# Optimization experiments

Hardware: AMD Instinct MI355X
Metric: run time of the kernel (lower is better)

The kernel has to match this reference:

```python
import jax, jax.numpy as jnp
import numpy as np

D = 256; NH = 8; NLEV = 4; NPTS = 4; DH = D // NH
DFFN = 1024; B = 8; LQ = 900
SHAPES = np.array([[100, 100], [50, 50], [25, 25], [13, 13]], dtype=np.int64)
STARTS = np.concatenate([[0], np.cumsum(SHAPES[:, 0] * SHAPES[:, 1])[:-1]]).astype(np.int64)
LEN = int((SHAPES[:, 0] * SHAPES[:, 1]).sum())


def _ln(x, w, b, eps=1e-5):
    m = x.mean(-1, keepdims=True)
    v = ((x - m) ** 2).mean(-1, keepdims=True)
    return (x - m) / jnp.sqrt(v + eps) * w + b


def _msdeform(q, ref, src, val_w, val_b, off_w, off_b, aw_w, aw_b, op_w, op_b):
    # Multi-scale deformable attention (Deformable DETR core), grid_sample
    # bilinear / zeros padding / align_corners=False semantics.
    Bq, Lq = q.shape[0], q.shape[1]
    value = (src @ val_w + val_b).reshape(Bq, -1, NH, DH)
    off = (q @ off_w + off_b).reshape(Bq, Lq, NH, NLEV, NPTS, 2)
    aw = jax.nn.softmax((q @ aw_w + aw_b).reshape(Bq, Lq, NH, NLEV * NPTS), -1)
    aw = aw.reshape(Bq, Lq, NH, NLEV, NPTS)
    norm = jnp.asarray(SHAPES[:, ::-1].copy(), dtype=q.dtype)  # (W_l, H_l)
    loc = ref[:, :, None, :, None, :] + off / norm[None, None, None, :, None, :]
    out = jnp.zeros((Bq, Lq, NH, DH), q.dtype)
    for l in range(NLEV):
        Hl, Wl = int(SHAPES[l, 0]), int(SHAPES[l, 1]); s = int(STARTS[l])
        v = value[:, s:s + Hl * Wl]                  # [B, Hl*Wl, NH, DH]
        lx = loc[:, :, :, l, :, 0] * Wl - 0.5        # align_corners=False pixel coords
        ly = loc[:, :, :, l, :, 1] * Hl - 0.5        # [B, Lq, NH, NPTS]
        x0 = jnp.floor(lx); y0 = jnp.floor(ly)
        fx = lx - x0; fy = ly - y0
        x0 = x0.astype(jnp.int32); y0 = y0.astype(jnp.int32)
        samp = jnp.zeros((Bq, Lq, NH, NPTS, DH), q.dtype)
        for dx, dy in ((0, 0), (1, 0), (0, 1), (1, 1)):
            xi = x0 + dx; yi = y0 + dy
            w = (fx if dx else 1.0 - fx) * (fy if dy else 1.0 - fy)
            valid = (xi >= 0) & (xi < Wl) & (yi >= 0) & (yi < Hl)
            idx = jnp.clip(yi, 0, Hl - 1) * Wl + jnp.clip(xi, 0, Wl - 1)
            idx_f = idx.transpose(0, 1, 3, 2).reshape(Bq, Lq * NPTS, NH)
            g = jnp.take_along_axis(v, idx_f[..., None], axis=1)
            g = g.reshape(Bq, Lq, NPTS, NH, DH).transpose(0, 1, 3, 2, 4)
            samp = samp + jnp.where(valid, w, 0.0)[..., None] * g
        out = out + jnp.sum(samp * aw[:, :, :, l, :, None], axis=3)
    return out.reshape(Bq, Lq, D) @ op_w + op_b


def _forward(tgt, query_pos, reference_points, src, qkv_w, qkv_b, out_w, out_b,
             ln2_w, ln2_b, val_w, val_b, off_w, off_b, aw_w, aw_b, op_w, op_b,
             ln1_w, ln1_b, w1, b1, w2, b2, ln3_w, ln3_b):
    Bq, Lq, _ = tgt.shape
    # --- self attention: q=k=tgt+pos, value=tgt (eval mode, no dropout) ---
    q = tgt + query_pos
    wq, wk, wv = qkv_w[:, :D], qkv_w[:, D:2 * D], qkv_w[:, 2 * D:]
    bq, bk, bv = qkv_b[:D], qkv_b[D:2 * D], qkv_b[2 * D:]
    qh = (q @ wq + bq).reshape(Bq, Lq, NH, DH)
    kh = (q @ wk + bk).reshape(Bq, Lq, NH, DH)
    vh = (tgt @ wv + bv).reshape(Bq, Lq, NH, DH)
    scores = jnp.einsum('bqhd,bkhd->bhqk', qh, kh) / jnp.sqrt(jnp.asarray(DH, tgt.dtype))
    attn = jax.nn.softmax(scores, -1)
    sa = jnp.einsum('bhqk,bkhd->bqhd', attn, vh).reshape(Bq, Lq, D) @ out_w + out_b
    tgt = _ln(tgt + sa, ln2_w, ln2_b)
    # --- multi-scale deformable cross attention ---
    ca = _msdeform(tgt + query_pos, reference_points, src,
                   val_w, val_b, off_w, off_b, aw_w, aw_b, op_w, op_b)
    tgt = _ln(tgt + ca, ln1_w, ln1_b)
    # --- FFN ---
    ff = jax.nn.relu(tgt @ w1 + b1) @ w2 + b2
    return _ln(tgt + ff, ln3_w, ln3_b)


def setup_inputs():
    key = jax.random.key(0)
    ks = jax.random.split(key, 16)
    s = 0.02
    return {
        'tgt': jax.random.normal(ks[0], (B, LQ, D), jnp.float32),
        'query_pos': jax.random.normal(ks[1], (B, LQ, D), jnp.float32),
        'reference_points': jax.random.uniform(ks[2], (B, LQ, NLEV, 2), jnp.float32),
        'src': jax.random.normal(ks[3], (B, LEN, D), jnp.float32),
        'spatial_shapes': jnp.asarray(SHAPES),
        'level_start_index': jnp.asarray(STARTS),
        'qkv_w': jax.random.normal(ks[4], (D, 3 * D), jnp.float32) * s,
        'qkv_b': jnp.zeros((3 * D,), jnp.float32),
        'out_w': jax.random.normal(ks[5], (D, D), jnp.float32) * s,
        'out_b': jnp.zeros((D,), jnp.float32),
        'ln2_w': jnp.ones((D,), jnp.float32), 'ln2_b': jnp.zeros((D,), jnp.float32),
        'val_w': jax.random.normal(ks[6], (D, D), jnp.float32) * s,
        'val_b': jnp.zeros((D,), jnp.float32),
        'off_w': jax.random.normal(ks[7], (D, NH * NLEV * NPTS * 2), jnp.float32) * s,
        'off_b': jax.random.normal(ks[8], (NH * NLEV * NPTS * 2,), jnp.float32) * 0.5,
        'aw_w': jax.random.normal(ks[9], (D, NH * NLEV * NPTS), jnp.float32) * s,
        'aw_b': jnp.zeros((NH * NLEV * NPTS,), jnp.float32),
        'op_w': jax.random.normal(ks[10], (D, D), jnp.float32) * s,
        'op_b': jnp.zeros((D,), jnp.float32),
        'ln1_w': jnp.ones((D,), jnp.float32), 'ln1_b': jnp.zeros((D,), jnp.float32),
        'w1': jax.random.normal(ks[11], (D, DFFN), jnp.float32) * s,
        'b1': jnp.zeros((DFFN,), jnp.float32),
        'w2': jax.random.normal(ks[12], (DFFN, D), jnp.float32) * s,
        'b2': jnp.zeros((D,), jnp.float32),
        'ln3_w': jnp.ones((D,), jnp.float32), 'ln3_b': jnp.zeros((D,), jnp.float32),
    }


def reference(tgt, query_pos, reference_points, src, spatial_shapes, level_start_index,
              qkv_w, qkv_b, out_w, out_b, ln2_w, ln2_b, val_w, val_b, off_w, off_b,
              aw_w, aw_b, op_w, op_b, ln1_w, ln1_b, w1, b1, w2, b2, ln3_w, ln3_b):
    return _forward(tgt, query_pos, reference_points, src, qkv_w, qkv_b, out_w, out_b,
                    ln2_w, ln2_b, val_w, val_b, off_w, off_b, aw_w, aw_b, op_w, op_b,
                    ln1_w, ln1_b, w1, b1, w2, b2, ln3_w, ln3_b)
```

## Files before the change

kernel.cpp:

```cpp
#include <hip/hip_runtime.h>
#include <math.h>

#define Dm    256
#define NHm   8
#define DHm   32
#define NLEVm 4
#define NPTSm 4
#define DFFNm 1024
#define Bm    8
#define LQm   900
#define LENm  13294
#define MQ    (Bm * LQm)
#define MV    (Bm * LENm)
#define MQP   7296
#define MVP   106368
#define LQP   960

typedef __attribute__((ext_vector_type(8))) short short8;
typedef __attribute__((ext_vector_type(4))) float f32x4;

__device__ __forceinline__ unsigned short f2bf(float f) {
    unsigned int b = __float_as_uint(f);
    unsigned int r = (b + 0x7FFFu + ((b >> 16) & 1u)) >> 16;
    return (unsigned short)r;
}
__device__ __forceinline__ float bf2f(unsigned short u) {
    return __uint_as_float(((unsigned int)u) << 16);
}

__global__ __launch_bounds__(256) void prep0(const float* __restrict__ tgt,
                                             const float* __restrict__ qpos,
                                             unsigned short* __restrict__ tgtb,
                                             unsigned short* __restrict__ qb,
                                             int n4, int n4pad) {
    int i = blockIdx.x * blockDim.x + threadIdx.x;
    int stride = gridDim.x * blockDim.x;
    for (; i < n4pad; i += stride) {
        ushort4 ut, uq;
        if (i < n4) {
            float4 x = reinterpret_cast<const float4*>(tgt)[i];
            float4 y = reinterpret_cast<const float4*>(qpos)[i];
            ut.x = f2bf(x.x); ut.y = f2bf(x.y); ut.z = f2bf(x.z); ut.w = f2bf(x.w);
            uq.x = f2bf(x.x + y.x); uq.y = f2bf(x.y + y.y);
            uq.z = f2bf(x.z + y.z); uq.w = f2bf(x.w + y.w);
        } else {
            ut.x = ut.y = ut.z = ut.w = 0;
            uq.x = uq.y = uq.z = uq.w = 0;
        }
        reinterpret_cast<ushort4*>(tgtb)[i] = ut;
        reinterpret_cast<ushort4*>(qb)[i] = uq;
    }
}

__device__ __forceinline__ void wt_tile(const float* __restrict__ W,
                                        unsigned short* __restrict__ BT,
                                        int N, int K, int n0, int k0, int t,
                                        float (*tile)[65]) {
    #pragma unroll
    for (int r0 = 0; r0 < 64; r0 += 16) {
        int r = r0 + (t >> 4);
        int c = (t & 15) * 4;
        float4 v = *reinterpret_cast<const float4*>(W + (size_t)(k0 + r) * N + n0 + c);
        tile[r][c + 0] = v.x; tile[r][c + 1] = v.y; tile[r][c + 2] = v.z; tile[r][c + 3] = v.w;
    }
    __syncthreads();
    #pragma unroll
    for (int s = t; s < 512; s += 256) {
        int r = s >> 3, c8 = (s & 7) * 8;
        short8 u;
        #pragma unroll
        for (int j = 0; j < 8; ++j) u[j] = (short)f2bf(tile[c8 + j][r]);
        *reinterpret_cast<short8*>(BT + (size_t)(n0 + r) * K + k0 + c8) = u;
    }
}

__global__ __launch_bounds__(256) void wt_all(
        const float* __restrict__ qkv_w, const float* __restrict__ out_w,
        const float* __restrict__ val_w, const float* __restrict__ off_w,
        const float* __restrict__ aw_w,  const float* __restrict__ op_w,
        const float* __restrict__ w1,    const float* __restrict__ w2,
        unsigned short* __restrict__ BT_qkv, unsigned short* __restrict__ BT_out,
        unsigned short* __restrict__ BT_val, unsigned short* __restrict__ BT_off,
        unsigned short* __restrict__ BT_aw,  unsigned short* __restrict__ BT_op,
        unsigned short* __restrict__ BT_w1,  unsigned short* __restrict__ BT_w2) {
    __shared__ float tile[64][65];
    int bid = blockIdx.x;
    int t = threadIdx.x;
    const float* W; unsigned short* BT; int N, K, idx;
    if      (bid < 48)  { W = qkv_w; BT = BT_qkv; N = 768;  K = 256;  idx = bid; }
    else if (bid < 64)  { W = out_w; BT = BT_out; N = 256;  K = 256;  idx = bid - 48; }
    else if (bid < 80)  { W = val_w; BT = BT_val; N = 256;  K = 256;  idx = bid - 64; }
    else if (bid < 96)  { W = off_w; BT = BT_off; N = 256;  K = 256;  idx = bid - 80; }
    else if (bid < 104) { W = aw_w;  BT = BT_aw;  N = 128;  K = 256;  idx = bid - 96; }
    else if (bid < 120) { W = op_w;  BT = BT_op;  N = 256;  K = 256;  idx = bid - 104; }
    else if (bid < 184) { W = w1;    BT = BT_w1;  N = 1024; K = 256;  idx = bid - 120; }
    else                { W = w2;    BT = BT_w2;  N = 256;  K = 1024; idx = bid - 184; }
    int nt = N / 64;
    int n0 = (idx % nt) * 64, k0 = (idx / nt) * 64;
    wt_tile(W, BT, N, K, n0, k0, t, tile);
}

__device__ __forceinline__ void mfma_step(const unsigned short* Ac, const unsigned short* Bc,
                                          int wr, int wc, int l, f32x4 acc[4][4]) {
    short8 af[4], bfr[4];
    #pragma unroll
    for (int m = 0; m < 4; ++m)
        af[m] = *(const short8*)(Ac + (wr + m * 16 + (l & 15)) * 32 + (l >> 4) * 8);
    #pragma unroll
    for (int n = 0; n < 4; ++n)
        bfr[n] = *(const short8*)(Bc + (wc + n * 16 + (l & 15)) * 32 + (l >> 4) * 8);
    #pragma unroll
    for (int m = 0; m < 4; ++m)
        #pragma unroll
        for (int n = 0; n < 4; ++n)
            acc[m][n] = __builtin_amdgcn_mfma_f32_16x16x32_bf16(af[m], bfr[n], acc[m][n], 0, 0, 0);
}

template <int RELU, int OBF>
__global__ __launch_bounds__(256) void bgemm(int M, int N, int K,
        const unsigned short* __restrict__ A,
        const unsigned short* __restrict__ BT,
        const float* __restrict__ bias, const float* __restrict__ bias2,
        float* __restrict__ Cf, float* __restrict__ Cf2,
        unsigned short* __restrict__ Cb, int ldc) {
    __shared__ __align__(16) unsigned short As[2][128 * 32];
    __shared__ __align__(16) unsigned short Bs[2][128 * 32];
    int t = threadIdx.x;
    int l = t & 63;
    int w = t >> 6;
    int row0 = blockIdx.x * 128, col0 = blockIdx.y * 128;
    int wr = (w >> 1) * 64, wc = (w & 1) * 64;
    f32x4 acc[4][4];
    #pragma unroll
    for (int m = 0; m < 4; ++m)
        #pragma unroll
        for (int n = 0; n < 4; ++n) acc[m][n] = (f32x4){0.f, 0.f, 0.f, 0.f};

    int s0 = t, s1 = t + 256;
    const unsigned short* Ag = A + (size_t)row0 * K;
    const unsigned short* Bg = BT + (size_t)col0 * K;
    const unsigned short* a0p = Ag + (size_t)(s0 >> 2) * K + (s0 & 3) * 8;
    const unsigned short* a1p = Ag + (size_t)(s1 >> 2) * K + (s1 & 3) * 8;
    const unsigned short* b0p = Bg + (size_t)(s0 >> 2) * K + (s0 & 3) * 8;
    const unsigned short* b1p = Bg + (size_t)(s1 >> 2) * K + (s1 & 3) * 8;

    short8 ra0 = *(const short8*)(a0p);
    short8 ra1 = *(const short8*)(a1p);
    short8 rb0 = *(const short8*)(b0p);
    short8 rb1 = *(const short8*)(b1p);

    int cur = 0;
    for (int k0 = 0; k0 < K; k0 += 32) {
        unsigned short* Ac = As[cur];
        unsigned short* Bc = Bs[cur];
        *(short8*)(Ac + s0 * 8) = ra0;
        *(short8*)(Ac + s1 * 8) = ra1;
        *(short8*)(Bc + s0 * 8) = rb0;
        *(short8*)(Bc + s1 * 8) = rb1;
        if (k0 + 32 < K) {
            ra0 = *(const short8*)(a0p + k0 + 32);
            ra1 = *(const short8*)(a1p + k0 + 32);
            rb0 = *(const short8*)(b0p + k0 + 32);
            rb1 = *(const short8*)(b1p + k0 + 32);
        }
        __syncthreads();
        mfma_step(Ac, Bc, wr, wc, l, acc);
        cur ^= 1;
    }

    int cr = (l >> 4) * 4;
    int cc = l & 15;
    #pragma unroll
    for (int m = 0; m < 4; ++m) {
        #pragma unroll
        for (int n = 0; n < 4; ++n) {
            int col = col0 + wc + n * 16 + cc;
            if (OBF == 3) {
                float bv = (col < 256) ? bias[col] : bias2[col - 256];
                #pragma unroll
                for (int j = 0; j < 4; ++j) {
                    int r = row0 + wr + m * 16 + cr + j;
                    if (r < M) {
                        float v = acc[m][n][j] + bv;
                        if (col < 256) Cf[(size_t)r * 256 + col] = v;
                        else           Cf2[(size_t)r * 128 + (col - 256)] = v;
                    }
                }
            } else {
                float bv = bias[col];
                #pragma unroll
                for (int j = 0; j < 4; ++j) {
                    int r = row0 + wr + m * 16 + cr + j;
                    if (r < M) {
                        float v = acc[m][n][j] + bv;
                        if (RELU) v = fmaxf(v, 0.f);
                        if (OBF) Cb[(size_t)r * ldc + col] = f2bf(v);
                        else     Cf[(size_t)r * ldc + col] = v;
                    }
                }
            }
        }
    }
}

__global__ __launch_bounds__(256) void fused_gemms(
        const float* __restrict__ src, const unsigned short* __restrict__ BT_val,
        const float* __restrict__ val_b, unsigned short* __restrict__ value_bf,
        const unsigned short* __restrict__ Qbf, const unsigned short* __restrict__ BT_qkv,
        const float* __restrict__ qkv_b, unsigned short* __restrict__ qk_bf,
        const unsigned short* __restrict__ tgt_bf, unsigned short* __restrict__ Vt) {
    __shared__ __align__(16) unsigned short As[2][128 * 32];
    __shared__ __align__(16) unsigned short Bs[2][128 * 32];
    int bid = blockIdx.x;
    int t = threadIdx.x;

    if (bid >= 2004) {
        int i = (bid - 2004) * 256 + t;
        int row = i / 60, c = 900 + (i % 60);
        Vt[(size_t)row * LQP + c] = 0;
        return;
    }

    int l = t & 63, w = t >> 6;
    int wr = (w >> 1) * 64, wc = (w & 1) * 64;
    int s0 = t, s1 = t + 256;
    f32x4 acc[4][4];
    #pragma unroll
    for (int m = 0; m < 4; ++m)
        #pragma unroll
        for (int n = 0; n < 4; ++n) acc[m][n] = (f32x4){0.f, 0.f, 0.f, 0.f};
    int cr = (l >> 4) * 4;
    int cc = l & 15;

    if (bid < 1662) {
        int row0 = (bid % 831) * 128, col0 = (bid / 831) * 128;
        int r0c = min(row0 + (s0 >> 2), MV - 1);
        int r1c = min(row0 + (s1 >> 2), MV - 1);
        const float* a0p = src + (size_t)r0c * 256 + (s0 & 3) * 8;
        const float* a1p = src + (size_t)r1c * 256 + (s1 & 3) * 8;
        const unsigned short* Bg = BT_val + (size_t)col0 * 256;
        const unsigned short* b0p = Bg + (size_t)(s0 >> 2) * 256 + (s0 & 3) * 8;
        const unsigned short* b1p = Bg + (size_t)(s1 >> 2) * 256 + (s1 & 3) * 8;

        float4 fa0 = *(const float4*)(a0p);
        float4 fa1 = *(const float4*)(a0p + 4);
        float4 fb0 = *(const float4*)(a1p);
        float4 fb1 = *(const float4*)(a1p + 4);
        short8 rb0 = *(const short8*)(b0p);
        short8 rb1 = *(const short8*)(b1p);

        int cur = 0;
        for (int k0 = 0; k0 < 256; k0 += 32) {
            unsigned short* Ac = As[cur];
            unsigned short* Bc = Bs[cur];
            short8 ra0, ra1;
            ra0[0] = (short)f2bf(fa0.x); ra0[1] = (short)f2bf(fa0.y);
            ra0[2] = (short)f2bf(fa0.z); ra0[3] = (short)f2bf(fa0.w);
            ra0[4] = (short)f2bf(fa1.x); ra0[5] = (short)f2bf(fa1.y);
            ra0[6] = (short)f2bf(fa1.z); ra0[7] = (short)f2bf(fa1.w);
            ra1[0] = (short)f2bf(fb0.x); ra1[1] = (short)f2bf(fb0.y);
            ra1[2] = (short)f2bf(fb0.z); ra1[3] = (short)f2bf(fb0.w);
            ra1[4] = (short)f2bf(fb1.x); ra1[5] = (short)f2bf(fb1.y);
            ra1[6] = (short)f2bf(fb1.z); ra1[7] = (short)f2bf(fb1.w);
            *(short8*)(Ac + s0 * 8) = ra0;
            *(short8*)(Ac + s1 * 8) = ra1;
            *(short8*)(Bc + s0 * 8) = rb0;
            *(short8*)(Bc + s1 * 8) = rb1;
            if (k0 + 32 < 256) {
                fa0 = *(const float4*)(a0p + k0 + 32);
                fa1 = *(const float4*)(a0p + k0 + 36);
                fb0 = *(const float4*)(a1p + k0 + 32);
                fb1 = *(const float4*)(a1p + k0 + 36);
                rb0 = *(const short8*)(b0p + k0 + 32);
                rb1 = *(const short8*)(b1p + k0 + 32);
            }
            __syncthreads();
            mfma_step(Ac, Bc, wr, wc, l, acc);
            cur ^= 1;
        }
        #pragma unroll
        for (int m = 0; m < 4; ++m) {
            #pragma unroll
            for (int n = 0; n < 4; ++n) {
                int col = col0 + wc + n * 16 + cc;
                float bv = val_b[col];
                #pragma unroll
                for (int j = 0; j < 4; ++j) {
                    int r = row0 + wr + m * 16 + cr + j;
                    if (r < MV)
                        value_bf[(size_t)r * 256 + col] = f2bf(acc[m][n][j] + bv);
                }
            }
        }
    } else {
        bool is_qk = (bid < 1890);
        int idx = is_qk ? (bid - 1662) : (bid - 1890);
        int row0 = (idx % 57) * 128;
        int col0 = (idx / 57) * 128;
        const unsigned short* A  = is_qk ? Qbf : tgt_bf;
        const unsigned short* BT = is_qk ? BT_qkv : (BT_qkv + 512 * 256);
        const float* bias        = is_qk ? qkv_b : (qkv_b + 512);

        const unsigned short* Ag = A + (size_t)row0 * 256;
        const unsigned short* Bg = BT + (size_t)col0 * 256;
        const unsigned short* a0p = Ag + (size_t)(s0 >> 2) * 256 + (s0 & 3) * 8;
        const unsigned short* a1p = Ag + (size_t)(s1 >> 2) * 256 + (s1 & 3) * 8;
        const unsigned short* b0p = Bg + (size_t)(s0 >> 2) * 256 + (s0 & 3) * 8;
        const unsigned short* b1p = Bg + (size_t)(s1 >> 2) * 256 + (s1 & 3) * 8;

        short8 ra0 = *(const short8*)(a0p);
        short8 ra1 = *(const short8*)(a1p);
        short8 rb0 = *(const short8*)(b0p);
        short8 rb1 = *(const short8*)(b1p);

        int cur = 0;
        for (int k0 = 0; k0 < 256; k0 += 32) {
            unsigned short* Ac = As[cur];
            unsigned short* Bc = Bs[cur];
            *(short8*)(Ac + s0 * 8) = ra0;
            *(short8*)(Ac + s1 * 8) = ra1;
            *(short8*)(Bc + s0 * 8) = rb0;
            *(short8*)(Bc + s1 * 8) = rb1;
            if (k0 + 32 < 256) {
                ra0 = *(const short8*)(a0p + k0 + 32);
                ra1 = *(const short8*)(a1p + k0 + 32);
                rb0 = *(const short8*)(b0p + k0 + 32);
                rb1 = *(const short8*)(b1p + k0 + 32);
            }
            __syncthreads();
            mfma_step(Ac, Bc, wr, wc, l, acc);
            cur ^= 1;
        }

        if (is_qk) {
            #pragma unroll
            for (int m = 0; m < 4; ++m) {
                #pragma unroll
                for (int n = 0; n < 4; ++n) {
                    int col = col0 + wc + n * 16 + cc;
                    float bv = bias[col];
                    #pragma unroll
                    for (int j = 0; j < 4; ++j) {
                        int r = row0 + wr + m * 16 + cr + j;
                        if (r < MQ)
                            qk_bf[(size_t)r * 512 + col] = f2bf(acc[m][n][j] + bv);
                    }
                }
            }
        } else {
            #pragma unroll
            for (int m = 0; m < 4; ++m) {
                #pragma unroll
                for (int n = 0; n < 4; ++n) {
                    int col = col0 + wc + n * 16 + cc;
                    float bv = bias[col];
                    int r0 = row0 + wr + m * 16 + cr;
                    if (r0 < MQ) {
                        int bb = r0 / 900;
                        int q = r0 - bb * 900;
                        ushort4 u;
                        u.x = f2bf(acc[m][n][0] + bv);
                        u.y = f2bf(acc[m][n][1] + bv);
                        u.z = f2bf(acc[m][n][2] + bv);
                        u.w = f2bf(acc[m][n][3] + bv);
                        *reinterpret_cast<ushort4*>(Vt + ((size_t)(bb * 256 + col)) * LQP + q) = u;
                    }
                }
            }
        }
    }
}

__global__ __launch_bounds__(256) void flash_mfma(const unsigned short* __restrict__ qk,
                                                  const unsigned short* __restrict__ vt,
                                                  unsigned short* __restrict__ out) {
    __shared__ unsigned short P_lds[4][16][72];
    int t = threadIdx.x;
    int l = t & 63, w = t >> 6;
    int lr = l & 15, lg = l >> 4;
    int qt = blockIdx.x, h = blockIdx.y, b = blockIdx.z;
    const float scale = 0.17677669529663687f;

    short8 qf = *(const short8*)(qk + (size_t)(b * LQm + qt * 64 + w * 16 + lr) * 512 + h * 32 + lg * 8);

    f32x4 accO[2];
    accO[0] = (f32x4){0.f, 0.f, 0.f, 0.f};
    accO[1] = (f32x4){0.f, 0.f, 0.f, 0.f};
    float mrow[4] = {-1e30f, -1e30f, -1e30f, -1e30f};
    float lrow[4] = {0.f, 0.f, 0.f, 0.f};
    const f32x4 zero = (f32x4){0.f, 0.f, 0.f, 0.f};
    const unsigned short* vtb = vt + ((size_t)(b * 256 + h * 32)) * LQP;

    for (int kt = 0; kt < 15; ++kt) {
        int k0 = kt * 64;
        f32x4 sfr[4];
        #pragma unroll
        for (int ks = 0; ks < 4; ++ks) {
            short8 kf = *(const short8*)(qk + (size_t)(b * LQm + k0 + ks * 16 + lr) * 512 + 256 + h * 32 + lg * 8);
            sfr[ks] = __builtin_amdgcn_mfma_f32_16x16x32_bf16(qf, kf, zero, 0, 0, 0);
        }
        float sv[4][4];
        #pragma unroll
        for (int ks = 0; ks < 4; ++ks) {
            bool valid = (k0 + ks * 16 + lr) < LQm;
            #pragma unroll
            for (int j = 0; j < 4; ++j)
                sv[ks][j] = valid ? sfr[ks][j] * scale : -1e30f;
        }
        float tm[4], newm[4], rr[4], ps[4];
        #pragma unroll
        for (int j = 0; j < 4; ++j)
            tm[j] = fmaxf(fmaxf(sv[0][j], sv[1][j]), fmaxf(sv[2][j], sv[3][j]));
        #pragma unroll
        for (int msk = 1; msk <= 8; msk <<= 1) {
            #pragma unroll
            for (int j = 0; j < 4; ++j) tm[j] = fmaxf(tm[j], __shfl_xor(tm[j], msk));
        }
        #pragma unroll
        for (int j = 0; j < 4; ++j) {
            newm[j] = fmaxf(mrow[j], tm[j]);
            rr[j] = __expf(mrow[j] - newm[j]);
            mrow[j] = newm[j];
            ps[j] = 0.f;
        }
        float pv[4][4];
        #pragma unroll
        for (int ks = 0; ks < 4; ++ks)
            #pragma unroll
            for (int j = 0; j < 4; ++j) {
                pv[ks][j] = __expf(sv[ks][j] - newm[j]);
                ps[j] += pv[ks][j];
            }
        #pragma unroll
        for (int msk = 1; msk <= 8; msk <<= 1) {
            #pragma unroll
            for (int j = 0; j < 4; ++j) ps[j] += __shfl_xor(ps[j], msk);
        }
        #pragma unroll
        for (int j = 0; j < 4; ++j) lrow[j] = lrow[j] * rr[j] + ps[j];
        #pragma unroll
        for (int n = 0; n < 2; ++n)
            #pragma unroll
            for (int j = 0; j < 4; ++j) accO[n][j] *= rr[j];
        #pragma unroll
        for (int ks = 0; ks < 4; ++ks)
            #pragma unroll
            for (int j = 0; j < 4; ++j)
                P_lds[w][lg * 4 + j][ks * 16 + lr] = f2bf(pv[ks][j]);
        #pragma unroll
        for (int kh2 = 0; kh2 < 2; ++kh2) {
            short8 pf = *(const short8*)(&P_lds[w][lr][kh2 * 32 + lg * 8]);
            #pragma unroll
            for (int n = 0; n < 2; ++n) {
                short8 vf = *(const short8*)(vtb + (size_t)(n * 16 + lr) * LQP + k0 + kh2 * 32 + lg * 8);
                accO[n] = __builtin_amdgcn_mfma_f32_16x16x32_bf16(pf, vf, accO[n], 0, 0, 0);
            }
        }
    }
    float inv[4];
    #pragma unroll
    for (int j = 0; j < 4; ++j) inv[j] = 1.0f / lrow[j];
    #pragma unroll
    for (int n = 0; n < 2; ++n)
        #pragma unroll
        for (int j = 0; j < 4; ++j) {
            int q = qt * 64 + w * 16 + lg * 4 + j;
            if (q < LQm)
                out[(size_t)(b * LQm + q) * 256 + h * 32 + n * 16 + lr] = f2bf(accO[n][j] * inv[j]);
        }
}

template <int DUAL, int QP>
__global__ __launch_bounds__(256) void add_ln_kernel(const float* __restrict__ x,
                                                     const float* __restrict__ r,
                                                     const float* __restrict__ w,
                                                     const float* __restrict__ b,
                                                     const float* __restrict__ qpos,
                                                     float* __restrict__ out,
                                                     unsigned short* __restrict__ outb,
                                                     unsigned short* __restrict__ outq) {
    int row = blockIdx.x * 4 + (threadIdx.x >> 6);
    int lane = threadIdx.x & 63;
    size_t i4 = (size_t)row * 64 + lane;
    float4 xv = reinterpret_cast<const float4*>(x)[i4];
    float4 rv = reinterpret_cast<const float4*>(r)[i4];
    float4 v = make_float4(xv.x + rv.x, xv.y + rv.y, xv.z + rv.z, xv.w + rv.w);
    float s = v.x + v.y + v.z + v.w;
    #pragma unroll
    for (int msk = 1; msk <= 32; msk <<= 1) s += __shfl_xor(s, msk);
    float mean = s * (1.0f / Dm);
    float4 dv = make_float4(v.x - mean, v.y - mean, v.z - mean, v.w - mean);
    float sq = dv.x * dv.x + dv.y * dv.y + dv.z * dv.z + dv.w * dv.w;
    #pragma unroll
    for (int msk = 1; msk <= 32; msk <<= 1) sq += __shfl_xor(sq, msk);
    float is = rsqrtf(sq * (1.0f / Dm) + 1e-5f);
    float4 wv = reinterpret_cast<const float4*>(w)[lane];
    float4 bv = reinterpret_cast<const float4*>(b)[lane];
    float4 res = make_float4(dv.x * is * wv.x + bv.x, dv.y * is * wv.y + bv.y,
                             dv.z * is * wv.z + bv.z, dv.w * is * wv.w + bv.w);
    reinterpret_cast<float4*>(out)[i4] = res;
    if (DUAL) {
        ushort4 u;
        u.x = f2bf(res.x); u.y = f2bf(res.y); u.z = f2bf(res.z); u.w = f2bf(res.w);
        reinterpret_cast<ushort4*>(outb)[i4] = u;
    }
    if (QP) {
        float4 qv = reinterpret_cast<const float4*>(qpos)[i4];
        ushort4 u;
        u.x = f2bf(res.x + qv.x); u.y = f2bf(res.y + qv.y);
        u.z = f2bf(res.z + qv.z); u.w = f2bf(res.w + qv.w);
        reinterpret_cast<ushort4*>(outq)[i4] = u;
    }
}

__global__ __launch_bounds__(256) void msdeform_kernel(const unsigned short* __restrict__ value,
                                                       const float* __restrict__ ref,
                                                       const float* __restrict__ off,
                                                       const float* __restrict__ awl,
                                                       unsigned short* __restrict__ out) {
    const int HL[4] = {100, 50, 25, 13};
    const int ST[4] = {0, 10000, 12500, 13125};
    __shared__ float lsx[4][128], lsy[4][128], wtab[4][128];
    __shared__ float2 ctab[4][512];
    int wv = threadIdx.x >> 6, lane = threadIdx.x & 63;
    int m = blockIdx.x * 4 + wv;
    int b = m / LQm;

    #pragma unroll
    for (int e = lane; e < 128; e += 64) {
        int lev = (e >> 2) & 3;
        float rx = ref[((size_t)m * NLEVm + lev) * 2 + 0];
        float ry = ref[((size_t)m * NLEVm + lev) * 2 + 1];
        float ox = off[(size_t)m * 256 + e * 2 + 0];
        float oy = off[(size_t)m * 256 + e * 2 + 1];
        float Wf = (float)HL[lev];
        lsx[wv][e] = (rx + ox / Wf) * Wf - 0.5f;
        lsy[wv][e] = (ry + oy / Wf) * Wf - 0.5f;
        wtab[wv][e] = awl[(size_t)m * 128 + e];
    }
    __syncthreads();
    if (lane < NHm) {
        int h = lane;
        float mx = -1e30f;
        #pragma unroll
        for (int i = 0; i < 16; i++) mx = fmaxf(mx, wtab[wv][h * 16 + i]);
        float s = 0.f;
        #pragma unroll
        for (int i = 0; i < 16; i++) {
            float e = __expf(wtab[wv][h * 16 + i] - mx);
            wtab[wv][h * 16 + i] = e; s += e;
        }
        float inv = 1.0f / s;
        #pragma unroll
        for (int i = 0; i < 16; i++) wtab[wv][h * 16 + i] *= inv;
    }
    __syncthreads();
    #pragma unroll
    for (int j = 0; j < 8; ++j) {
        int e2 = lane * 8 + j;
        int c = e2 & 3, e = e2 >> 2;
        int lev = (e >> 2) & 3;
        int Wl = HL[lev];
        float lx = lsx[wv][e], ly = lsy[wv][e];
        float x0f = floorf(lx), y0f = floorf(ly);
        float fx = lx - x0f, fy = ly - y0f;
        int dx = c & 1, dy = c >> 1;
        int xi = (int)x0f + dx, yi = (int)y0f + dy;
        bool valid = (xi >= 0) && (xi < Wl) && (yi >= 0) && (yi < Wl);
        float wc = valid ? ((dx ? fx : 1.0f - fx) * (dy ? fy : 1.0f - fy)) * wtab[wv][e] : 0.f;
        int xc = min(max(xi, 0), Wl - 1), yc = min(max(yi, 0), Wl - 1);
        int row = b * LENm + ST[lev] + yc * Wl + xc;
        ctab[wv][e2] = make_float2(__int_as_float(row), wc);
    }
    __syncthreads();
    int h = lane >> 3, dg = lane & 7;
    const unsigned short* basep = value + h * 32 + dg * 4;
    float a0 = 0.f, a1 = 0.f, a2 = 0.f, a3 = 0.f;
    #pragma unroll
    for (int i = 0; i < 16; ++i) {
        #pragma unroll
        for (int c = 0; c < 4; ++c) {
            float2 cc = ctab[wv][(h * 16 + i) * 4 + c];
            int row = __float_as_int(cc.x);
            float wc = cc.y;
            ushort4 v = *reinterpret_cast<const ushort4*>(basep + (size_t)row * 256);
            a0 += wc * bf2f(v.x); a1 += wc * bf2f(v.y);
            a2 += wc * bf2f(v.z); a3 += wc * bf2f(v.w);
        }
    }
    ushort4 o;
    o.x = f2bf(a0); o.y = f2bf(a1); o.z = f2bf(a2); o.w = f2bf(a3);
    *reinterpret_cast<ushort4*>(out + (size_t)m * 256 + h * 32 + dg * 4) = o;
}

extern "C" void kernel_launch(void* const* d_in, const int* in_sizes, int n_in,
                              void* d_out, int out_size, void* d_ws, size_t ws_size,
                              hipStream_t stream) {
    const float* tgt   = (const float*)d_in[0];
    const float* qpos  = (const float*)d_in[1];
    const float* refp  = (const float*)d_in[2];
    const float* src   = (const float*)d_in[3];
    const float* qkv_w = (const float*)d_in[6];
    const float* qkv_b = (const float*)d_in[7];
    const float* out_w = (const float*)d_in[8];
    const float* out_b = (const float*)d_in[9];
    const float* ln2_w = (const float*)d_in[10];
    const float* ln2_b = (const float*)d_in[11];
    const float* val_w = (const float*)d_in[12];
    const float* val_b = (const float*)d_in[13];
    const float* off_w = (const float*)d_in[14];
    const float* off_b = (const float*)d_in[15];
    const float* aw_w  = (const float*)d_in[16];
    const float* aw_b  = (const float*)d_in[17];
    const float* op_w  = (const float*)d_in[18];
    const float* op_b  = (const float*)d_in[19];
    const float* ln1_w = (const float*)d_in[20];
    const float* ln1_b = (const float*)d_in[21];
    const float* w1    = (const float*)d_in[22];
    const float* b1    = (const float*)d_in[23];
    const float* w2    = (const float*)d_in[24];
    const float* b2    = (const float*)d_in[25];
    const float* ln3_w = (const float*)d_in[26];
    const float* ln3_b = (const float*)d_in[27];

    char* base = (char*)d_ws;
    unsigned short* value_bf  = (unsigned short*)(base);
    unsigned short* hidden_bf = (unsigned short*)(base + 54460416);
    unsigned short* t2_bf     = (unsigned short*)(base + 54460416 + 14942208);
    unsigned short* qk_bf = (unsigned short*)(base + 108920832);
    float* offb = (float*)(base + 108920832);
    float* awb  = (float*)(base + 108920832 + 7372800);
    unsigned short* Vt = (unsigned short*)(base + 123666432);
    float* S1   = (float*)(base + 123666432);
    float* t1   = (float*)(base + 131039232);
    float* t2   = (float*)(base + 138412032);
    unsigned short* Qbf     = (unsigned short*)(base + 145784832);
    unsigned short* tgt_bf  = (unsigned short*)(base + 149520384);
    unsigned short* attn_bf = (unsigned short*)(base + 153255936);
    unsigned short* ca_bf   = (unsigned short*)(base + 156991488);
    unsigned short* BT_qkv  = (unsigned short*)(base + 160727040);
    unsigned short* BT_out  = BT_qkv + 768 * 256;
    unsigned short* BT_val  = BT_out + 256 * 256;
    unsigned short* BT_off  = BT_val + 256 * 256;
    unsigned short* BT_aw   = BT_off + 256 * 256;
    unsigned short* BT_op   = BT_aw + 128 * 256;
    unsigned short* BT_w1   = BT_op + 256 * 256;
    unsigned short* BT_w2   = BT_w1 + 1024 * 256;
    float* outp = (float*)d_out;

    dim3 blk(256);
    wt_all<<<dim3(248), blk, 0, stream>>>(qkv_w, out_w, val_w, off_w, aw_w, op_w, w1, w2,
                                          BT_qkv, BT_out, BT_val, BT_off, BT_aw, BT_op, BT_w1, BT_w2);
    prep0<<<dim3(1824), blk, 0, stream>>>(tgt, qpos, tgt_bf, Qbf, MQ * Dm / 4, MQP * Dm / 4);

    fused_gemms<<<dim3(2484), blk, 0, stream>>>(src, BT_val, val_b, value_bf,
                                                Qbf, BT_qkv, qkv_b, qk_bf, tgt_bf, Vt);

    flash_mfma<<<dim3(15, NHm, Bm), blk, 0, stream>>>(qk_bf, Vt, attn_bf);
    bgemm<0, 0><<<dim3(57, 2), blk, 0, stream>>>(MQ, 256, 256, attn_bf, BT_out, out_b, nullptr, S1, nullptr, nullptr, 256);
    add_ln_kernel<0, 1><<<dim3(1800), blk, 0, stream>>>(tgt, S1, ln2_w, ln2_b, qpos, t1, nullptr, Qbf);
    bgemm<0, 3><<<dim3(57, 3), blk, 0, stream>>>(MQ, 384, 256, Qbf, BT_off, off_b, aw_b, offb, awb, nullptr, 0);
    msdeform_kernel<<<dim3(1800), blk, 0, stream>>>(value_bf, refp, offb, awb, ca_bf);
    bgemm<0, 0><<<dim3(57, 2), blk, 0, stream>>>(MQ, 256, 256, ca_bf, BT_op, op_b, nullptr, S1, nullptr, nullptr, 256);
    add_ln_kernel<1, 0><<<dim3(1800), blk, 0, stream>>>(t1, S1, ln1_w, ln1_b, nullptr, t2, t2_bf, nullptr);
    bgemm<1, 1><<<dim3(57, 8), blk, 0, stream>>>(MQ, DFFNm, 256, t2_bf, BT_w1, b1, nullptr, nullptr, nullptr, hidden_bf, DFFNm);
    bgemm<0, 0><<<dim3(57, 2), blk, 0, stream>>>(MQ, 256, 1024, hidden_bf, BT_w2, b2, nullptr, S1, nullptr, nullptr, 256);
    add_ln_kernel<0, 0><<<dim3(1800), blk, 0, stream>>>(t2, S1, ln3_w, ln3_b, nullptr, outp, nullptr, nullptr);
}
```

Before: 251.4 us.

## Overlap value projection with self-attention chain via staged combo kernels

Splits the large value-projection GEMM (src @ val_w) into chunks and co-schedules each chunk inside a sequence of combo kernel launches. The same launches also run the self-attention pipeline stages: QKV projection, flash attention, out-projection, LN plus query_pos, and the offset/attention-weight GEMM. The goal is to fill idle CUs during the small, low-occupancy self-attention stages with independent value-GEMM tiles, and to fold the weight transpose and the input prep into one launch. The cost is a more complex heterogeneous block dispatch and a shared LDS size that may limit occupancy.

```diff
diff --git a/kernel.cpp b/kernel.cpp
--- a/kernel.cpp
+++ b/kernel.cpp
@@ -28,16 +28,46 @@
     return __uint_as_float(((unsigned int)u) << 16);
 }
 
-__global__ __launch_bounds__(256) void prep0(const float* __restrict__ tgt,
-                                             const float* __restrict__ qpos,
-                                             unsigned short* __restrict__ tgtb,
-                                             unsigned short* __restrict__ qb,
-                                             int n4, int n4pad) {
-    int i = blockIdx.x * blockDim.x + threadIdx.x;
-    int stride = gridDim.x * blockDim.x;
-    for (; i < n4pad; i += stride) {
+__device__ __forceinline__ void wt_tile(const float* __restrict__ W,
+                                        unsigned short* __restrict__ BT,
+                                        int N, int K, int n0, int k0, int t,
+                                        float (*tile)[65]) {
+    #pragma unroll
+    for (int r0 = 0; r0 < 64; r0 += 16) {
+        int r = r0 + (t >> 4);
+        int c = (t & 15) * 4;
+        float4 v = *reinterpret_cast<const float4*>(W + (size_t)(k0 + r) * N + n0 + c);
+        tile[r][c + 0] = v.x; tile[r][c + 1] = v.y; tile[r][c + 2] = v.z; tile[r][c + 3] = v.w;
+    }
+    __syncthreads();
+    #pragma unroll
+    for (int s = t; s < 512; s += 256) {
+        int r = s >> 3, c8 = (s & 7) * 8;
+        short8 u;
+        #pragma unroll
+        for (int j = 0; j < 8; ++j) u[j] = (short)f2bf(tile[c8 + j][r]);
+        *reinterpret_cast<short8*>(BT + (size_t)(n0 + r) * K + k0 + c8) = u;
+    }
+}
+
+__global__ __launch_bounds__(256) void wt_prep(
+        const float* __restrict__ qkv_w, const float* __restrict__ out_w,
+        const float* __restrict__ val_w, const float* __restrict__ off_w,
+        const float* __restrict__ aw_w,  const float* __restrict__ op_w,
+        const float* __restrict__ w1,    const float* __restrict__ w2,
+        unsigned short* __restrict__ BT_qkv, unsigned short* __restrict__ BT_out,
+        unsigned short* __restrict__ BT_val, unsigned short* __restrict__ BT_off,
+        unsigned short* __restrict__ BT_aw,  unsigned short* __restrict__ BT_op,
+        unsigned short* __restrict__ BT_w1,  unsigned short* __restrict__ BT_w2,
+        const float* __restrict__ tgt, const float* __restrict__ qpos,
+        unsigned short* __restrict__ tgtb, unsigned short* __restrict__ qb) {
+    __shared__ float tile[64][65];
+    int bid = blockIdx.x;
+    int t = threadIdx.x;
+    if (bid >= 248) {
+        int i = (bid - 248) * 256 + t;
         ushort4 ut, uq;
-        if (i < n4) {
+        if (i < MQ * 64) {
             float4 x = reinterpret_cast<const float4*>(tgt)[i];
             float4 y = reinterpret_cast<const float4*>(qpos)[i];
             ut.x = f2bf(x.x); ut.y = f2bf(x.y); ut.z = f2bf(x.z); ut.w = f2bf(x.w);
@@ -49,43 +79,8 @@
         }
         reinterpret_cast<ushort4*>(tgtb)[i] = ut;
         reinterpret_cast<ushort4*>(qb)[i] = uq;
-    }
-}
-
-__device__ __forceinline__ void wt_tile(const float* __restrict__ W,
-                                        unsigned short* __restrict__ BT,
-                                        int N, int K, int n0, int k0, int t,
-                                        float (*tile)[65]) {
-    #pragma unroll
-    for (int r0 = 0; r0 < 64; r0 += 16) {
-        int r = r0 + (t >> 4);
-        int c = (t & 15) * 4;
-        float4 v = *reinterpret_cast<const float4*>(W + (size_t)(k0 + r) * N + n0 + c);
-        tile[r][c + 0] = v.x; tile[r][c + 1] = v.y; tile[r][c + 2] = v.z; tile[r][c + 3] = v.w;
-    }
-    __syncthreads();
-    #pragma unroll
-    for (int s = t; s < 512; s += 256) {
-        int r = s >> 3, c8 = (s & 7) * 8;
-        short8 u;
-        #pragma unroll
-        for (int j = 0; j < 8; ++j) u[j] = (short)f2bf(tile[c8 + j][r]);
-        *reinterpret_cast<short8*>(BT + (size_t)(n0 + r) * K + k0 + c8) = u;
-    }
-}
-
-__global__ __launch_bounds__(256) void wt_all(
-        const float* __restrict__ qkv_w, const float* __restrict__ out_w,
-        const float* __restrict__ val_w, const float* __restrict__ off_w,
-        const float* __restrict__ aw_w,  const float* __restrict__ op_w,
-        const float* __restrict__ w1,    const float* __restrict__ w2,
-        unsigned short* __restrict__ BT_qkv, unsigned short* __restrict__ BT_out,
-        unsigned short* __restrict__ BT_val, unsigned short* __restrict__ BT_off,
-        unsigned short* __restrict__ BT_aw,  unsigned short* __restrict__ BT_op,
-        unsigned short* __restrict__ BT_w1,  unsigned short* __restrict__ BT_w2) {
-    __shared__ float tile[64][65];
-    int bid = blockIdx.x;
-    int t = threadIdx.x;
+        return;
+    }
     const float* W; unsigned short* BT; int N, K, idx;
     if      (bid < 48)  { W = qkv_w; BT = BT_qkv; N = 768;  K = 256;  idx = bid; }
     else if (bid < 64)  { W = out_w; BT = BT_out; N = 256;  K = 256;  idx = bid - 48; }
@@ -100,8 +95,8 @@
     wt_tile(W, BT, N, K, n0, k0, t, tile);
 }
 
-__device__ __forceinline__ void mfma_step(const unsigned short* Ac, const unsigned short* Bc,
-                                          int wr, int wc, int l, f32x4 acc[4][4]) {
+__device__ __forceinline__ void mfma_tilestep(const unsigned short* Ac, const unsigned short* Bc,
+                                              int wr, int wc, int l, f32x4 acc[4][4]) {
     short8 af[4], bfr[4];
     #pragma unroll
     for (int m = 0; m < 4; ++m)
@@ -114,15 +109,380 @@
         #pragma unroll
         for (int n = 0; n < 4; ++n)
             acc[m][n] = __builtin_amdgcn_mfma_f32_16x16x32_bf16(af[m], bfr[n], acc[m][n], 0, 0, 0);
+}
+
+__device__ __forceinline__ void bf16_mainloop(int t, const unsigned short* __restrict__ Ag,
+                                              const unsigned short* __restrict__ Bg,
+                                              unsigned short* Sh, f32x4 acc[4][4]) {
+    int l = t & 63, w = t >> 6;
+    int wr = (w >> 1) * 64, wc = (w & 1) * 64;
+    int s0 = t, s1 = t + 256;
+    const unsigned short* a0p = Ag + (size_t)(s0 >> 2) * 256 + (s0 & 3) * 8;
+    const unsigned short* a1p = Ag + (size_t)(s1 >> 2) * 256 + (s1 & 3) * 8;
+    const unsigned short* b0p = Bg + (size_t)(s0 >> 2) * 256 + (s0 & 3) * 8;
+    const unsigned short* b1p = Bg + (size_t)(s1 >> 2) * 256 + (s1 & 3) * 8;
+    short8 ra0 = *(const short8*)(a0p);
+    short8 ra1 = *(const short8*)(a1p);
+    short8 rb0 = *(const short8*)(b0p);
+    short8 rb1 = *(const short8*)(b1p);
+    int cur = 0;
+    for (int k0 = 0; k0 < 256; k0 += 32) {
+        unsigned short* Ac = Sh + cur * 4096;
+        unsigned short* Bc = Sh + 8192 + cur * 4096;
+        *(short8*)(Ac + s0 * 8) = ra0;
+        *(short8*)(Ac + s1 * 8) = ra1;
+        *(short8*)(Bc + s0 * 8) = rb0;
+        *(short8*)(Bc + s1 * 8) = rb1;
+        if (k0 + 32 < 256) {
+            ra0 = *(const short8*)(a0p + k0 + 32);
+            ra1 = *(const short8*)(a1p + k0 + 32);
+            rb0 = *(const short8*)(b0p + k0 + 32);
+            rb1 = *(const short8*)(b1p + k0 + 32);
+        }
+        __syncthreads();
+        mfma_tilestep(Ac, Bc, wr, wc, l, acc);
+        cur ^= 1;
+    }
+}
+
+__device__ __forceinline__ void value_tile(int vbid, int t, const float* __restrict__ src,
+        const unsigned short* __restrict__ BT_val, const float* __restrict__ val_b,
+        unsigned short* __restrict__ value_bf, unsigned short* Sh) {
+    int l = t & 63, w = t >> 6;
+    int wr = (w >> 1) * 64, wc = (w & 1) * 64;
+    int row0 = (vbid % 831) * 128, col0 = (vbid / 831) * 128;
+    f32x4 acc[4][4];
+    #pragma unroll
+    for (int m = 0; m < 4; ++m)
+        #pragma unroll
+        for (int n = 0; n < 4; ++n) acc[m][n] = (f32x4){0.f, 0.f, 0.f, 0.f};
+    int s0 = t, s1 = t + 256;
+    int r0c = min(row0 + (s0 >> 2), MV - 1);
+    int r1c = min(row0 + (s1 >> 2), MV - 1);
+    const float* a0p = src + (size_t)r0c * 256 + (s0 & 3) * 8;
+    const float* a1p = src + (size_t)r1c * 256 + (s1 & 3) * 8;
+    const unsigned short* Bg = BT_val + (size_t)col0 * 256;
+    const unsigned short* b0p = Bg + (size_t)(s0 >> 2) * 256 + (s0 & 3) * 8;
+    const unsigned short* b1p = Bg + (size_t)(s1 >> 2) * 256 + (s1 & 3) * 8;
+    float4 fa0 = *(const float4*)(a0p);
+    float4 fa1 = *(const float4*)(a0p + 4);
+    float4 fb0 = *(const float4*)(a1p);
+    float4 fb1 = *(const float4*)(a1p + 4);
+    short8 rb0 = *(const short8*)(b0p);
+    short8 rb1 = *(const short8*)(b1p);
+    int cur = 0;
+    for (int k0 = 0; k0 < 256; k0 += 32) {
+        unsigned short* Ac = Sh + cur * 4096;
+        unsigned short* Bc = Sh + 8192 + cur * 4096;
+        short8 ra0, ra1;
+        ra0[0] = (short)f2bf(fa0.x); ra0[1] = (short)f2bf(fa0.y);
+        ra0[2] = (short)f2bf(fa0.z); ra0[3] = (short)f2bf(fa0.w);
+        ra0[4] = (short)f2bf(fa1.x); ra0[5] = (short)f2bf(fa1.y);
+        ra0[6] = (short)f2bf(fa1.z); ra0[7] = (short)f2bf(fa1.w);
+        ra1[0] = (short)f2bf(fb0.x); ra1[1] = (short)f2bf(fb0.y);
+        ra1[2] = (short)f2bf(fb0.z); ra1[3] = (short)f2bf(fb0.w);
+        ra1[4] = (short)f2bf(fb1.x); ra1[5] = (short)f2bf(fb1.y);
+        ra1[6] = (short)f2bf(fb1.z); ra1[7] = (short)f2bf(fb1.w);
+        *(short8*)(Ac + s0 * 8) = ra0;
+        *(short8*)(Ac + s1 * 8) = ra1;
+        *(short8*)(Bc + s0 * 8) = rb0;
+        *(short8*)(Bc + s1 * 8) = rb1;
+        if (k0 + 32 < 256) {
+            fa0 = *(const float4*)(a0p + k0 + 32);
+            fa1 = *(const float4*)(a0p + k0 + 36);
+            fb0 = *(const float4*)(a1p + k0 + 32);
+            fb1 = *(const float4*)(a1p + k0 + 36);
+            rb0 = *(const short8*)(b0p + k0 + 32);
+            rb1 = *(const short8*)(b1p + k0 + 32);
+        }
+        __syncthreads();
+        mfma_tilestep(Ac, Bc, wr, wc, l, acc);
+        cur ^= 1;
+    }
+    int cr = (l >> 4) * 4, cc = l & 15;
+    #pragma unroll
+    for (int m = 0; m < 4; ++m) {
+        #pragma unroll
+        for (int n = 0; n < 4; ++n) {
+            int col = col0 + wc + n * 16 + cc;
+            float bv = val_b[col];
+            #pragma unroll
+            for (int j = 0; j < 4; ++j) {
+                int r = row0 + wr + m * 16 + cr + j;
+                if (r < MV)
+                    value_bf[(size_t)r * 256 + col] = f2bf(acc[m][n][j] + bv);
+            }
+        }
+    }
+}
+
+__device__ __forceinline__ void flash_block(int sid, int t,
+        const unsigned short* __restrict__ qk, const unsigned short* __restrict__ vt,
+        unsigned short* __restrict__ out, unsigned short* P_lds ) {
+    int l = t & 63, w = t >> 6;
+    int lr = l & 15, lg = l >> 4;
+    int qt = sid % 15, h = (sid / 15) % 8, b = sid / 120;
+    const float scale = 0.17677669529663687f;
+    unsigned short* Pw = P_lds + w * 1152;
+
+    short8 qf = *(const short8*)(qk + (size_t)(b * LQm + qt * 64 + w * 16 + lr) * 512 + h * 32 + lg * 8);
+
+    f32x4 accO[2];
+    accO[0] = (f32x4){0.f, 0.f, 0.f, 0.f};
+    accO[1] = (f32x4){0.f, 0.f, 0.f, 0.f};
+    float mrow[4] = {-1e30f, -1e30f, -1e30f, -1e30f};
+    float lrow[4] = {0.f, 0.f, 0.f, 0.f};
+    const f32x4 zero = (f32x4){0.f, 0.f, 0.f, 0.f};
+    const unsigned short* vtb = vt + ((size_t)(b * 256 + h * 32)) * LQP;
+
+    for (int kt = 0; kt < 15; ++kt) {
+        int k0 = kt * 64;
+        f32x4 sfr[4];
+        #pragma unroll
+        for (int ks = 0; ks < 4; ++ks) {
+            short8 kf = *(const short8*)(qk + (size_t)(b * LQm + k0 + ks * 16 + lr) * 512 + 256 + h * 32 + lg * 8);
+            sfr[ks] = __builtin_amdgcn_mfma_f32_16x16x32_bf16(qf, kf, zero, 0, 0, 0);
+        }
+        float sv[4][4];
+        #pragma unroll
+        for (int ks = 0; ks < 4; ++ks) {
+            bool valid = (k0 + ks * 16 + lr) < LQm;
+            #pragma unroll
+            for (int j = 0; j < 4; ++j)
+                sv[ks][j] = valid ? sfr[ks][j] * scale : -1e30f;
+        }
+        float tm[4], newm[4], rr[4], ps[4];
+        #pragma unroll
+        for (int j = 0; j < 4; ++j)
+            tm[j] = fmaxf(fmaxf(sv[0][j], sv[1][j]), fmaxf(sv[2][j], sv[3][j]));
+        #pragma unroll
+        for (int msk = 1; msk <= 8; msk <<= 1) {
+            #pragma unroll
+            for (int j = 0; j < 4; ++j) tm[j] = fmaxf(tm[j], __shfl_xor(tm[j], msk));
+        }
+        #pragma unroll
+        for (int j = 0; j < 4; ++j) {
+            newm[j] = fmaxf(mrow[j], tm[j]);
+            rr[j] = __expf(mrow[j] - newm[j]);
+            mrow[j] = newm[j];
+            ps[j] = 0.f;
+        }
+        float pv[4][4];
+        #pragma unroll
+        for (int ks = 0; ks < 4; ++ks)
+            #pragma unroll
+            for (int j = 0; j < 4; ++j) {
+                pv[ks][j] = __expf(sv[ks][j] - newm[j]);
+                ps[j] += pv[ks][j];
+            }
+        #pragma unroll
+        for (int msk = 1; msk <= 8; msk <<= 1) {
+            #pragma unroll
+            for (int j = 0; j < 4; ++j) ps[j] += __shfl_xor(ps[j], msk);
+        }
+        #pragma unroll
+        for (int j = 0; j < 4; ++j) lrow[j] = lrow[j] * rr[j] + ps[j];
+        #pragma unroll
+        for (int n = 0; n < 2; ++n)
+            #pragma unroll
+            for (int j = 0; j < 4; ++j) accO[n][j] *= rr[j];
+        #pragma unroll
+        for (int ks = 0; ks < 4; ++ks)
+            #pragma unroll
+            for (int j = 0; j < 4; ++j)
+                Pw[(lg * 4 + j) * 72 + ks * 16 + lr] = f2bf(pv[ks][j]);
+        #pragma unroll
+        for (int kh2 = 0; kh2 < 2; ++kh2) {
+            short8 pf = *(const short8*)(Pw + lr * 72 + kh2 * 32 + lg * 8);
+            #pragma unroll
+            for (int n = 0; n < 2; ++n) {
+                short8 vf = *(const short8*)(vtb + (size_t)(n * 16 + lr) * LQP + k0 + kh2 * 32 + lg * 8);
+                accO[n] = __builtin_amdgcn_mfma_f32_16x16x32_bf16(pf, vf, accO[n], 0, 0, 0);
+            }
+        }
+    }
+    float inv[4];
+    #pragma unroll
+    for (int j = 0; j < 4; ++j) inv[j] = 1.0f / lrow[j];
+    #pragma unroll
+    for (int n = 0; n < 2; ++n)
+        #pragma unroll
+        for (int j = 0; j < 4; ++j) {
+            int q = qt * 64 + w * 16 + lg * 4 + j;
+            if (q < LQm)
+                out[(size_t)(b * LQm + q) * 256 + h * 32 + n * 16 + lr] = f2bf(accO[n][j] * inv[j]);
+        }
+}
+
+__device__ __forceinline__ void ln_block(int sid, int t, const float* __restrict__ x,
+        const float* __restrict__ r, const float* __restrict__ w, const float* __restrict__ b,
+        const float* __restrict__ qpos, float* __restrict__ out,
+        unsigned short* __restrict__ outq) {
+    int row = sid * 4 + (t >> 6);
+    int lane = t & 63;
+    size_t i4 = (size_t)row * 64 + lane;
+    float4 xv = reinterpret_cast<const float4*>(x)[i4];
+    float4 rv = reinterpret_cast<const float4*>(r)[i4];
+    float4 v = make_float4(xv.x + rv.x, xv.y + rv.y, xv.z + rv.z, xv.w + rv.w);
+    float s = v.x + v.y + v.z + v.w;
+    #pragma unroll
+    for (int msk = 1; msk <= 32; msk <<= 1) s += __shfl_xor(s, msk);
+    float mean = s * (1.0f / Dm);
+    float4 dv = make_float4(v.x - mean, v.y - mean, v.z - mean, v.w - mean);
+    float sq = dv.x * dv.x + dv.y * dv.y + dv.z * dv.z + dv.w * dv.w;
+    #pragma unroll
+    for (int msk = 1; msk <= 32; msk <<= 1) sq += __shfl_xor(sq, msk);
+    float is = rsqrtf(sq * (1.0f / Dm) + 1e-5f);
+    float4 wv = reinterpret_cast<const float4*>(w)[lane];
+    float4 bv = reinterpret_cast<const float4*>(b)[lane];
+    float4 res = make_float4(dv.x * is * wv.x + bv.x, dv.y * is * wv.y + bv.y,
+                             dv.z * is * wv.z + bv.z, dv.w * is * wv.w + bv.w);
+    reinterpret_cast<float4*>(out)[i4] = res;
+    float4 qv = reinterpret_cast<const float4*>(qpos)[i4];
+    ushort4 u;
+    u.x = f2bf(res.x + qv.x); u.y = f2bf(res.y + qv.y);
+    u.z = f2bf(res.z + qv.z); u.w = f2bf(res.w + qv.w);
+    reinterpret_cast<ushort4*>(outq)[i4] = u;
+}
+
+template <int SEC>
+__global__ __launch_bounds__(256) void combo(int vlo, int vcnt,
+        const float* __restrict__ src, const unsigned short* __restrict__ BT_val,
+        const float* __restrict__ val_b, unsigned short* __restrict__ value_bf,
+        const unsigned short* __restrict__ Qbf, const unsigned short* __restrict__ BT_qkv,
+        const float* __restrict__ qkv_b, unsigned short* __restrict__ qk_bf,
+        const unsigned short* __restrict__ tgt_bf, unsigned short* __restrict__ Vt,
+        const unsigned short* __restrict__ attn_bf, const unsigned short* __restrict__ BT_out,
+        const float* __restrict__ out_b, float* __restrict__ S1,
+        const float* __restrict__ tgt, const float* __restrict__ qpos,
+        const float* __restrict__ ln2_w, const float* __restrict__ ln2_b,
+        float* __restrict__ t1, unsigned short* __restrict__ Qbf_out,
+        const unsigned short* __restrict__ BT_off, const float* __restrict__ off_b,
+        const float* __restrict__ aw_b, float* __restrict__ offb, float* __restrict__ awb,
+        unsigned short* __restrict__ attn_out) {
+    __shared__ __align__(16) unsigned short Sh[16384];
+    int bid = blockIdx.x;
+    int t = threadIdx.x;
+    if (bid < vcnt) {
+        value_tile(vlo + bid, t, src, BT_val, val_b, value_bf, Sh);
+        return;
+    }
+    int sid = bid - vcnt;
+    int l = t & 63, w = t >> 6;
+    int wr = (w >> 1) * 64, wc = (w & 1) * 64;
+    int cr = ((l >> 4)) * 4, cc = l & 15;
+
+    if (SEC == 0) {
+        if (sid < 342) {
+            bool is_qk = (sid < 228);
+            int idx = is_qk ? sid : (sid - 228);
+            int row0 = (idx % 57) * 128, col0 = (idx / 57) * 128;
+            const unsigned short* A  = is_qk ? Qbf : tgt_bf;
+            const unsigned short* BT = is_qk ? BT_qkv : (BT_qkv + 512 * 256);
+            const float* bias        = is_qk ? qkv_b : (qkv_b + 512);
+            f32x4 acc[4][4];
+            #pragma unroll
+            for (int m = 0; m < 4; ++m)
+                #pragma unroll
+                for (int n = 0; n < 4; ++n) acc[m][n] = (f32x4){0.f, 0.f, 0.f, 0.f};
+            bf16_mainloop(t, A + (size_t)row0 * 256, BT + (size_t)col0 * 256, Sh, acc);
+            if (is_qk) {
+                #pragma unroll
+                for (int m = 0; m < 4; ++m)
+                    #pragma unroll
+                    for (int n = 0; n < 4; ++n) {
+                        int col = col0 + wc + n * 16 + cc;
+                        float bv = bias[col];
+                        #pragma unroll
+                        for (int j = 0; j < 4; ++j) {
+                            int r = row0 + wr + m * 16 + cr + j;
+                            if (r < MQ)
+                                qk_bf[(size_t)r * 512 + col] = f2bf(acc[m][n][j] + bv);
+                        }
+                    }
+            } else {
+                #pragma unroll
+                for (int m = 0; m < 4; ++m)
+                    #pragma unroll
+                    for (int n = 0; n < 4; ++n) {
+                        int col = col0 + wc + n * 16 + cc;
+                        float bv = bias[col];
+                        int r0 = row0 + wr + m * 16 + cr;
+                        if (r0 < MQ) {
+                            int bb = r0 / 900;
+                            int q = r0 - bb * 900;
+                            ushort4 u;
+                            u.x = f2bf(acc[m][n][0] + bv);
+                            u.y = f2bf(acc[m][n][1] + bv);
+                            u.z = f2bf(acc[m][n][2] + bv);
+                            u.w = f2bf(acc[m][n][3] + bv);
+                            *reinterpret_cast<ushort4*>(Vt + ((size_t)(bb * 256 + col)) * LQP + q) = u;
+                        }
+                    }
+            }
+        } else {
+            int i = (sid - 342) * 256 + t;
+            int row = i / 60, c = 900 + (i % 60);
+            Vt[(size_t)row * LQP + c] = 0;
+        }
+    } else if (SEC == 1) {
+        flash_block(sid, t, qk_bf, Vt, attn_out, Sh);
+    } else if (SEC == 2) {
+        int row0 = (sid % 57) * 128, col0 = (sid / 57) * 128;
+        f32x4 acc[4][4];
+        #pragma unroll
+        for (int m = 0; m < 4; ++m)
+            #pragma unroll
+            for (int n = 0; n < 4; ++n) acc[m][n] = (f32x4){0.f, 0.f, 0.f, 0.f};
+        bf16_mainloop(t, attn_bf + (size_t)row0 * 256, BT_out + (size_t)col0 * 256, Sh, acc);
+        #pragma unroll
+        for (int m = 0; m < 4; ++m)
+            #pragma unroll
+            for (int n = 0; n < 4; ++n) {
+                int col = col0 + wc + n * 16 + cc;
+                float bv = out_b[col];
+                #pragma unroll
+                for (int j = 0; j < 4; ++j) {
+                    int r = row0 + wr + m * 16 + cr + j;
+                    if (r < MQ)
+                        S1[(size_t)r * 256 + col] = acc[m][n][j] + bv;
+                }
+            }
+    } else if (SEC == 3) {
+        ln_block(sid, t, tgt, S1, ln2_w, ln2_b, qpos, t1, Qbf_out);
+    } else {
+        int row0 = (sid % 57) * 128, col0 = (sid / 57) * 128;
+        f32x4 acc[4][4];
+        #pragma unroll
+        for (int m = 0; m < 4; ++m)
+            #pragma unroll
+            for (int n = 0; n < 4; ++n) acc[m][n] = (f32x4){0.f, 0.f, 0.f, 0.f};
+        bf16_mainloop(t, Qbf + (size_t)row0 * 256, BT_off + (size_t)col0 * 256, Sh, acc);
+        #pragma unroll
+        for (int m = 0; m < 4; ++m)
+            #pragma unroll
+            for (int n = 0; n < 4; ++n) {
+                int col = col0 + wc + n * 16 + cc;
+                float bv = (col < 256) ? off_b[col] : aw_b[col - 256];
+                #pragma unroll
+                for (int j = 0; j < 4; ++j) {
+                    int r = row0 + wr + m * 16 + cr + j;
+                    if (r < MQ) {
+                        float v = acc[m][n][j] + bv;
+                        if (col < 256) offb[(size_t)r * 256 + col] = v;
+                        else           awb[(size_t)r * 128 + (col - 256)] = v;
+                    }
+                }
+            }
+    }
 }
 
 template <int RELU, int OBF>
 __global__ __launch_bounds__(256) void bgemm(int M, int N, int K,
         const unsigned short* __restrict__ A,
         const unsigned short* __restrict__ BT,
-        const float* __restrict__ bias, const float* __restrict__ bias2,
-        float* __restrict__ Cf, float* __restrict__ Cf2,
-        unsigned short* __restrict__ Cb, int ldc) {
+        const float* __restrict__ bias,
+        float* __restrict__ Cf, unsigned short* __restrict__ Cb, int ldc) {
     __shared__ __align__(16) unsigned short As[2][128 * 32];
     __shared__ __align__(16) unsigned short Bs[2][128 * 32];
     int t = threadIdx.x;
@@ -164,7 +524,7 @@
             rb1 = *(const short8*)(b1p + k0 + 32);
         }
         __syncthreads();
-        mfma_step(Ac, Bc, wr, wc, l, acc);
+        mfma_tilestep(Ac, Bc, wr, wc, l, acc);
         cur ^= 1;
     }
 
@@ -175,310 +535,28 @@
         #pragma unroll
         for (int n = 0; n < 4; ++n) {
             int col = col0 + wc + n * 16 + cc;
-            if (OBF == 3) {
-                float bv = (col < 256) ? bias[col] : bias2[col - 256];
-                #pragma unroll
-                for (int j = 0; j < 4; ++j) {
-                    int r = row0 + wr + m * 16 + cr + j;
-                    if (r < M) {
-                        float v = acc[m][n][j] + bv;
-                        if (col < 256) Cf[(size_t)r * 256 + col] = v;
-                        else           Cf2[(size_t)r * 128 + (col - 256)] = v;
-                    }
-                }
-            } else {
-                float bv = bias[col];
-                #pragma unroll
-                for (int j = 0; j < 4; ++j) {
-                    int r = row0 + wr + m * 16 + cr + j;
-                    if (r < M) {
-                        float v = acc[m][n][j] + bv;
-                        if (RELU) v = fmaxf(v, 0.f);
-                        if (OBF) Cb[(size_t)r * ldc + col] = f2bf(v);
-                        else     Cf[(size_t)r * ldc + col] = v;
-                    }
+            float bv = bias[col];
+            #pragma unroll
+            for (int j = 0; j < 4; ++j) {
+                int r = row0 + wr + m * 16 + cr + j;
+                if (r < M) {
+                    float v = acc[m][n][j] + bv;
+                    if (RELU) v = fmaxf(v, 0.f);
+                    if (OBF) Cb[(size_t)r * ldc + col] = f2bf(v);
+                    else     Cf[(size_t)r * ldc + col] = v;
                 }
             }
         }
     }
 }
 
-__global__ __launch_bounds__(256) void fused_gemms(
-        const float* __restrict__ src, const unsigned short* __restrict__ BT_val,
-        const float* __restrict__ val_b, unsigned short* __restrict__ value_bf,
-        const unsigned short* __restrict__ Qbf, const unsigned short* __restrict__ BT_qkv,
-        const float* __restrict__ qkv_b, unsigned short* __restrict__ qk_bf,
-        const unsigned short* __restrict__ tgt_bf, unsigned short* __restrict__ Vt) {
-    __shared__ __align__(16) unsigned short As[2][128 * 32];
-    __shared__ __align__(16) unsigned short Bs[2][128 * 32];
-    int bid = blockIdx.x;
-    int t = threadIdx.x;
-
-    if (bid >= 2004) {
-        int i = (bid - 2004) * 256 + t;
-        int row = i / 60, c = 900 + (i % 60);
-        Vt[(size_t)row * LQP + c] = 0;
-        return;
-    }
-
-    int l = t & 63, w = t >> 6;
-    int wr = (w >> 1) * 64, wc = (w & 1) * 64;
-    int s0 = t, s1 = t + 256;
-    f32x4 acc[4][4];
-    #pragma unroll
-    for (int m = 0; m < 4; ++m)
-        #pragma unroll
-        for (int n = 0; n < 4; ++n) acc[m][n] = (f32x4){0.f, 0.f, 0.f, 0.f};
-    int cr = (l >> 4) * 4;
-    int cc = l & 15;
-
-    if (bid < 1662) {
-        int row0 = (bid % 831) * 128, col0 = (bid / 831) * 128;
-        int r0c = min(row0 + (s0 >> 2), MV - 1);
-        int r1c = min(row0 + (s1 >> 2), MV - 1);
-        const float* a0p = src + (size_t)r0c * 256 + (s0 & 3) * 8;
-        const float* a1p = src + (size_t)r1c * 256 + (s1 & 3) * 8;
-        const unsigned short* Bg = BT_val + (size_t)col0 * 256;
-        const unsigned short* b0p = Bg + (size_t)(s0 >> 2) * 256 + (s0 & 3) * 8;
-        const unsigned short* b1p = Bg + (size_t)(s1 >> 2) * 256 + (s1 & 3) * 8;
-
-        float4 fa0 = *(const float4*)(a0p);
-        float4 fa1 = *(const float4*)(a0p + 4);
-        float4 fb0 = *(const float4*)(a1p);
-        float4 fb1 = *(const float4*)(a1p + 4);
-        short8 rb0 = *(const short8*)(b0p);
-        short8 rb1 = *(const short8*)(b1p);
-
-        int cur = 0;
-        for (int k0 = 0; k0 < 256; k0 += 32) {
-            unsigned short* Ac = As[cur];
-            unsigned short* Bc = Bs[cur];
-            short8 ra0, ra1;
-            ra0[0] = (short)f2bf(fa0.x); ra0[1] = (short)f2bf(fa0.y);
-            ra0[2] = (short)f2bf(fa0.z); ra0[3] = (short)f2bf(fa0.w);
-            ra0[4] = (short)f2bf(fa1.x); ra0[5] = (short)f2bf(fa1.y);
-            ra0[6] = (short)f2bf(fa1.z); ra0[7] = (short)f2bf(fa1.w);
-            ra1[0] = (short)f2bf(fb0.x); ra1[1] = (short)f2bf(fb0.y);
-            ra1[2] = (short)f2bf(fb0.z); ra1[3] = (short)f2bf(fb0.w);
-            ra1[4] = (short)f2bf(fb1.x); ra1[5] = (short)f2bf(fb1.y);
-            ra1[6] = (short)f2bf(fb1.z); ra1[7] = (short)f2bf(fb1.w);
-            *(short8*)(Ac + s0 * 8) = ra0;
-            *(short8*)(Ac + s1 * 8) = ra1;
-            *(short8*)(Bc + s0 * 8) = rb0;
-            *(short8*)(Bc + s1 * 8) = rb1;
-            if (k0 + 32 < 256) {
-                fa0 = *(const float4*)(a0p + k0 + 32);
-                fa1 = *(const float4*)(a0p + k0 + 36);
-                fb0 = *(const float4*)(a1p + k0 + 32);
-                fb1 = *(const float4*)(a1p + k0 + 36);
-                rb0 = *(const short8*)(b0p + k0 + 32);
-                rb1 = *(const short8*)(b1p + k0 + 32);
-            }
-            __syncthreads();
-            mfma_step(Ac, Bc, wr, wc, l, acc);
-            cur ^= 1;
-        }
-        #pragma unroll
-        for (int m = 0; m < 4; ++m) {
-            #pragma unroll
-            for (int n = 0; n < 4; ++n) {
-                int col = col0 + wc + n * 16 + cc;
-                float bv = val_b[col];
-                #pragma unroll
-                for (int j = 0; j < 4; ++j) {
-                    int r = row0 + wr + m * 16 + cr + j;
-                    if (r < MV)
-                        value_bf[(size_t)r * 256 + col] = f2bf(acc[m][n][j] + bv);
-                }
-            }
-        }
-    } else {
-        bool is_qk = (bid < 1890);
-        int idx = is_qk ? (bid - 1662) : (bid - 1890);
-        int row0 = (idx % 57) * 128;
-        int col0 = (idx / 57) * 128;
-        const unsigned short* A  = is_qk ? Qbf : tgt_bf;
-        const unsigned short* BT = is_qk ? BT_qkv : (BT_qkv + 512 * 256);
-        const float* bias        = is_qk ? qkv_b : (qkv_b + 512);
-
-        const unsigned short* Ag = A + (size_t)row0 * 256;
-        const unsigned short* Bg = BT + (size_t)col0 * 256;
-        const unsigned short* a0p = Ag + (size_t)(s0 >> 2) * 256 + (s0 & 3) * 8;
-        const unsigned short* a1p = Ag + (size_t)(s1 >> 2) * 256 + (s1 & 3) * 8;
-        const unsigned short* b0p = Bg + (size_t)(s0 >> 2) * 256 + (s0 & 3) * 8;
-        const unsigned short* b1p = Bg + (size_t)(s1 >> 2) * 256 + (s1 & 3) * 8;
-
-        short8 ra0 = *(const short8*)(a0p);
-        short8 ra1 = *(const short8*)(a1p);
-        short8 rb0 = *(const short8*)(b0p);
-        short8 rb1 = *(const short8*)(b1p);
-
-        int cur = 0;
-        for (int k0 = 0; k0 < 256; k0 += 32) {
-            unsigned short* Ac = As[cur];
-            unsigned short* Bc = Bs[cur];
-            *(short8*)(Ac + s0 * 8) = ra0;
-            *(short8*)(Ac + s1 * 8) = ra1;
-            *(short8*)(Bc + s0 * 8) = rb0;
-            *(short8*)(Bc + s1 * 8) = rb1;
-            if (k0 + 32 < 256) {
-                ra0 = *(const short8*)(a0p + k0 + 32);
-                ra1 = *(const short8*)(a1p + k0 + 32);
-                rb0 = *(const short8*)(b0p + k0 + 32);
-                rb1 = *(const short8*)(b1p + k0 + 32);
-            }
-            __syncthreads();
-            mfma_step(Ac, Bc, wr, wc, l, acc);
-            cur ^= 1;
-        }
-
-        if (is_qk) {
-            #pragma unroll
-            for (int m = 0; m < 4; ++m) {
-                #pragma unroll
-                for (int n = 0; n < 4; ++n) {
-                    int col = col0 + wc + n * 16 + cc;
-                    float bv = bias[col];
-                    #pragma unroll
-                    for (int j = 0; j < 4; ++j) {
-                        int r = row0 + wr + m * 16 + cr + j;
-                        if (r < MQ)
-                            qk_bf[(size_t)r * 512 + col] = f2bf(acc[m][n][j] + bv);
-                    }
-                }
-            }
-        } else {
-            #pragma unroll
-            for (int m = 0; m < 4; ++m) {
-                #pragma unroll
-                for (int n = 0; n < 4; ++n) {
-                    int col = col0 + wc + n * 16 + cc;
-                    float bv = bias[col];
-                    int r0 = row0 + wr + m * 16 + cr;
-                    if (r0 < MQ) {
-                        int bb = r0 / 900;
-                        int q = r0 - bb * 900;
-                        ushort4 u;
-                        u.x = f2bf(acc[m][n][0] + bv);
-                        u.y = f2bf(acc[m][n][1] + bv);
-                        u.z = f2bf(acc[m][n][2] + bv);
-                        u.w = f2bf(acc[m][n][3] + bv);
-                        *reinterpret_cast<ushort4*>(Vt + ((size_t)(bb * 256 + col)) * LQP + q) = u;
-                    }
-                }
-            }
-        }
-    }
-}
-
-__global__ __launch_bounds__(256) void flash_mfma(const unsigned short* __restrict__ qk,
-                                                  const unsigned short* __restrict__ vt,
-                                                  unsigned short* __restrict__ out) {
-    __shared__ unsigned short P_lds[4][16][72];
-    int t = threadIdx.x;
-    int l = t & 63, w = t >> 6;
-    int lr = l & 15, lg = l >> 4;
-    int qt = blockIdx.x, h = blockIdx.y, b = blockIdx.z;
-    const float scale = 0.17677669529663687f;
-
-    short8 qf = *(const short8*)(qk + (size_t)(b * LQm + qt * 64 + w * 16 + lr) * 512 + h * 32 + lg * 8);
-
-    f32x4 accO[2];
-    accO[0] = (f32x4){0.f, 0.f, 0.f, 0.f};
-    accO[1] = (f32x4){0.f, 0.f, 0.f, 0.f};
-    float mrow[4] = {-1e30f, -1e30f, -1e30f, -1e30f};
-    float lrow[4] = {0.f, 0.f, 0.f, 0.f};
-    const f32x4 zero = (f32x4){0.f, 0.f, 0.f, 0.f};
-    const unsigned short* vtb = vt + ((size_t)(b * 256 + h * 32)) * LQP;
-
-    for (int kt = 0; kt < 15; ++kt) {
-        int k0 = kt * 64;
-        f32x4 sfr[4];
-        #pragma unroll
-        for (int ks = 0; ks < 4; ++ks) {
-            short8 kf = *(const short8*)(qk + (size_t)(b * LQm + k0 + ks * 16 + lr) * 512 + 256 + h * 32 + lg * 8);
-            sfr[ks] = __builtin_amdgcn_mfma_f32_16x16x32_bf16(qf, kf, zero, 0, 0, 0);
-        }
-        float sv[4][4];
-        #pragma unroll
-        for (int ks = 0; ks < 4; ++ks) {
-            bool valid = (k0 + ks * 16 + lr) < LQm;
-            #pragma unroll
-            for (int j = 0; j < 4; ++j)
-                sv[ks][j] = valid ? sfr[ks][j] * scale : -1e30f;
-        }
-        float tm[4], newm[4], rr[4], ps[4];
-        #pragma unroll
-        for (int j = 0; j < 4; ++j)
-            tm[j] = fmaxf(fmaxf(sv[0][j], sv[1][j]), fmaxf(sv[2][j], sv[3][j]));
-        #pragma unroll
-        for (int msk = 1; msk <= 8; msk <<= 1) {
-            #pragma unroll
-            for (int j = 0; j < 4; ++j) tm[j] = fmaxf(tm[j], __shfl_xor(tm[j], msk));
-        }
-        #pragma unroll
-        for (int j = 0; j < 4; ++j) {
-            newm[j] = fmaxf(mrow[j], tm[j]);
-            rr[j] = __expf(mrow[j] - newm[j]);
-            mrow[j] = newm[j];
-            ps[j] = 0.f;
-        }
-        float pv[4][4];
-        #pragma unroll
-        for (int ks = 0; ks < 4; ++ks)
-            #pragma unroll
-            for (int j = 0; j < 4; ++j) {
-                pv[ks][j] = __expf(sv[ks][j] - newm[j]);
-                ps[j] += pv[ks][j];
-            }
-        #pragma unroll
-        for (int msk = 1; msk <= 8; msk <<= 1) {
-            #pragma unroll
-            for (int j = 0; j < 4; ++j) ps[j] += __shfl_xor(ps[j], msk);
-        }
-        #pragma unroll
-        for (int j = 0; j < 4; ++j) lrow[j] = lrow[j] * rr[j] + ps[j];
-        #pragma unroll
-        for (int n = 0; n < 2; ++n)
-            #pragma unroll
-            for (int j = 0; j < 4; ++j) accO[n][j] *= rr[j];
-        #pragma unroll
-        for (int ks = 0; ks < 4; ++ks)
-            #pragma unroll
-            for (int j = 0; j < 4; ++j)
-                P_lds[w][lg * 4 + j][ks * 16 + lr] = f2bf(pv[ks][j]);
-        #pragma unroll
-        for (int kh2 = 0; kh2 < 2; ++kh2) {
-            short8 pf = *(const short8*)(&P_lds[w][lr][kh2 * 32 + lg * 8]);
-            #pragma unroll
-            for (int n = 0; n < 2; ++n) {
-                short8 vf = *(const short8*)(vtb + (size_t)(n * 16 + lr) * LQP + k0 + kh2 * 32 + lg * 8);
-                accO[n] = __builtin_amdgcn_mfma_f32_16x16x32_bf16(pf, vf, accO[n], 0, 0, 0);
-            }
-        }
-    }
-    float inv[4];
-    #pragma unroll
-    for (int j = 0; j < 4; ++j) inv[j] = 1.0f / lrow[j];
-    #pragma unroll
-    for (int n = 0; n < 2; ++n)
-        #pragma unroll
-        for (int j = 0; j < 4; ++j) {
-            int q = qt * 64 + w * 16 + lg * 4 + j;
-            if (q < LQm)
-                out[(size_t)(b * LQm + q) * 256 + h * 32 + n * 16 + lr] = f2bf(accO[n][j] * inv[j]);
-        }
-}
-
-template <int DUAL, int QP>
+template <int DUAL>
 __global__ __launch_bounds__(256) void add_ln_kernel(const float* __restrict__ x,
                                                      const float* __restrict__ r,
                                                      const float* __restrict__ w,
                                                      const float* __restrict__ b,
-                                                     const float* __restrict__ qpos,
                                                      float* __restrict__ out,
-                                                     unsigned short* __restrict__ outb,
-                                                     unsigned short* __restrict__ outq) {
+                                                     unsigned short* __restrict__ outb) {
     int row = blockIdx.x * 4 + (threadIdx.x >> 6);
     int lane = threadIdx.x & 63;
     size_t i4 = (size_t)row * 64 + lane;
@@ -503,13 +581,6 @@
         ushort4 u;
         u.x = f2bf(res.x); u.y = f2bf(res.y); u.z = f2bf(res.z); u.w = f2bf(res.w);
         reinterpret_cast<ushort4*>(outb)[i4] = u;
-    }
-    if (QP) {
-        float4 qv = reinterpret_cast<const float4*>(qpos)[i4];
-        ushort4 u;
-        u.x = f2bf(res.x + qv.x); u.y = f2bf(res.y + qv.y);
-        u.z = f2bf(res.z + qv.z); u.w = f2bf(res.w + qv.w);
-        reinterpret_cast<ushort4*>(outq)[i4] = u;
     }
 }
 
@@ -649,21 +720,24 @@
     float* outp = (float*)d_out;
 
     dim3 blk(256);
-    wt_all<<<dim3(248), blk, 0, stream>>>(qkv_w, out_w, val_w, off_w, aw_w, op_w, w1, w2,
-                                          BT_qkv, BT_out, BT_val, BT_off, BT_aw, BT_op, BT_w1, BT_w2);
-    prep0<<<dim3(1824), blk, 0, stream>>>(tgt, qpos, tgt_bf, Qbf, MQ * Dm / 4, MQP * Dm / 4);
-
-    fused_gemms<<<dim3(2484), blk, 0, stream>>>(src, BT_val, val_b, value_bf,
-                                                Qbf, BT_qkv, qkv_b, qk_bf, tgt_bf, Vt);
-
-    flash_mfma<<<dim3(15, NHm, Bm), blk, 0, stream>>>(qk_bf, Vt, attn_bf);
-    bgemm<0, 0><<<dim3(57, 2), blk, 0, stream>>>(MQ, 256, 256, attn_bf, BT_out, out_b, nullptr, S1, nullptr, nullptr, 256);
-    add_ln_kernel<0, 1><<<dim3(1800), blk, 0, stream>>>(tgt, S1, ln2_w, ln2_b, qpos, t1, nullptr, Qbf);
-    bgemm<0, 3><<<dim3(57, 3), blk, 0, stream>>>(MQ, 384, 256, Qbf, BT_off, off_b, aw_b, offb, awb, nullptr, 0);
+    wt_prep<<<dim3(2072), blk, 0, stream>>>(qkv_w, out_w, val_w, off_w, aw_w, op_w, w1, w2,
+                                            BT_qkv, BT_out, BT_val, BT_off, BT_aw, BT_op, BT_w1, BT_w2,
+                                            tgt, qpos, tgt_bf, Qbf);
+
+    #define COMBO_ARGS src, BT_val, val_b, value_bf, Qbf, BT_qkv, qkv_b, qk_bf, tgt_bf, Vt, \
+                       attn_bf, BT_out, out_b, S1, tgt, qpos, ln2_w, ln2_b, t1, Qbf, \
+                       BT_off, off_b, aw_b, offb, awb, attn_bf
+    combo<0><<<dim3(333 + 822), blk, 0, stream>>>(0, 333, COMBO_ARGS);
+    combo<1><<<dim3(666 + 960), blk, 0, stream>>>(333, 666, COMBO_ARGS);
+    combo<2><<<dim3(332 + 114), blk, 0, stream>>>(999, 332, COMBO_ARGS);
+    combo<3><<<dim3(166 + 1800), blk, 0, stream>>>(1331, 166, COMBO_ARGS);
+    combo<4><<<dim3(165 + 171), blk, 0, stream>>>(1497, 165, COMBO_ARGS);
+    #undef COMBO_ARGS
+
     msdeform_kernel<<<dim3(1800), blk, 0, stream>>>(value_bf, refp, offb, awb, ca_bf);
-    bgemm<0, 0><<<dim3(57, 2), blk, 0, stream>>>(MQ, 256, 256, ca_bf, BT_op, op_b, nullptr, S1, nullptr, nullptr, 256);
-    add_ln_kernel<1, 0><<<dim3(1800), blk, 0, stream>>>(t1, S1, ln1_w, ln1_b, nullptr, t2, t2_bf, nullptr);
-    bgemm<1, 1><<<dim3(57, 8), blk, 0, stream>>>(MQ, DFFNm, 256, t2_bf, BT_w1, b1, nullptr, nullptr, nullptr, hidden_bf, DFFNm);
-    bgemm<0, 0><<<dim3(57, 2), blk, 0, stream>>>(MQ, 256, 1024, hidden_bf, BT_w2, b2, nullptr, S1, nullptr, nullptr, 256);
-    add_ln_kernel<0, 0><<<dim3(1800), blk, 0, stream>>>(t2, S1, ln3_w, ln3_b, nullptr, outp, nullptr, nullptr);
-}
+    bgemm<0, 0><<<dim3(57, 2), blk, 0, stream>>>(MQ, 256, 256, ca_bf, BT_op, op_b, S1, nullptr, 256);
+    add_ln_kernel<1><<<dim3(1800), blk, 0, stream>>>(t1, S1, ln1_w, ln1_b, t2, t2_bf);
+    bgemm<1, 1><<<dim3(57, 8), blk, 0, stream>>>(MQ, DFFNm, 256, t2_bf, BT_w1, b1, nullptr, hidden_bf, DFFNm);
+    bgemm<0, 0><<<dim3(57, 2), blk, 0, stream>>>(MQ, 256, 1024, hidden_bf, BT_w2, b2, S1, nullptr, 256);
+    add_ln_kernel<0><<<dim3(1800), blk, 0, stream>>>(t2, S1, ln3_w, ln3_b, outp, nullptr);
+}
```

Measured after the change: 259.7 us. 3.3% more time.
